# Optimization experiments

Measured on AMD Instinct MI355X. Metric: run time of the kernel, lower is better.

## Reference

```python
import jax, jax.numpy as jnp
import numpy as np

EPS = 1e-5

def _dynconv(x, w):
    # x: [B,C,H,W], w: [B,O,C,1,1] -> per-sample 1x1 conv == batched matmul
    return jnp.einsum('bchw,boc->bohw', x, w[:, :, :, 0, 0])

def _instance_norm(x):
    # InstanceNorm2d(affine=False): normalize over HxW per (b,c), biased var
    m = jnp.mean(x, axis=(2, 3), keepdims=True)
    v = jnp.var(x, axis=(2, 3), keepdims=True)
    return (x - m) / jnp.sqrt(v + EPS)

def setup_inputs() -> dict:
    key = jax.random.key(0)
    ks = jax.random.split(key, 10)
    B, C, O = 16, 128, 128
    hs = [128, 64, 32, 16, 8]
    inp = {}
    for i, h in enumerate(hs):
        inp[f'x{i+1}'] = jax.random.normal(ks[i], (B, C, h, h), dtype=jnp.float32)
        inp[f'l{i+1}fs'] = jax.random.normal(ks[5 + i], (B, O, C, 1, 1), dtype=jnp.float32)
    return inp

def reference(x1, x2, x3, x4, x5, l1fs, l2fs, l3fs, l4fs, l5fs):
    y1 = _instance_norm(_dynconv(x1, l1fs))
    y2 = _instance_norm(_dynconv(x2, l2fs))
    y3 = _instance_norm(_dynconv(x3, l3fs))
    y4 = _instance_norm(_dynconv(x4, l4fs))
    y5 = _dynconv(x5, l5fs)  # x5 is not normalized in the original
    return (y1, y2, y3, y4, y5)
```

## Files before the change

kernel.cpp:

```cpp
#include <hip/hip_runtime.h>
#include <hip/hip_bf16.h>

typedef float f32x4 __attribute__((ext_vector_type(4)));
typedef short s16x8 __attribute__((ext_vector_type(8)));
typedef short s16x4 __attribute__((ext_vector_type(4)));

static __device__ __forceinline__ short f2bf(float f) {
  union { __hip_bfloat16 h; short s; } u;
  u.h = __float2bfloat16(f);
  return u.s;
}
static __device__ __forceinline__ float bf2f(short s) {
  union { unsigned u; float f; } v;
  v.u = ((unsigned)(unsigned short)s) << 16;
  return v.f;
}
static __device__ __forceinline__ unsigned pack2(float a, float b) {
  return ((unsigned)(unsigned short)f2bf(a)) | (((unsigned)(unsigned short)f2bf(b)) << 16);
}
static __device__ __forceinline__ s16x8 pack8(f32x4 v0, f32x4 v1) {
  s16x8 r;
  r[0] = f2bf(v0.x); r[1] = f2bf(v0.y); r[2] = f2bf(v0.z); r[3] = f2bf(v0.w);
  r[4] = f2bf(v1.x); r[5] = f2bf(v1.y); r[6] = f2bf(v1.z); r[7] = f2bf(v1.w);
  return r;
}

#define GRAW_SZ   (4 * 16 * 16384)
#define MX_BASE   GRAW_SZ
#define MX_SZ     (4 * 16 * 128)
#define MEAN_BASE (MX_BASE + MX_SZ)
#define RSTD_BASE (MEAN_BASE + MX_SZ)

__global__ __launch_bounds__(256, 3) void k_gram(
    const float* __restrict__ x0, const float* __restrict__ x1,
    const float* __restrict__ x2, const float* __restrict__ x3,
    float* __restrict__ graw, float* __restrict__ mxraw) {
  const int bid = blockIdx.x;
  const float* xp; int s, b, ch, L; long long N;
  if (bid < 512)      { s = 0; b = bid >> 5; ch = bid & 31; xp = x0; N = 16384; L = 512; }
  else if (bid < 640) { int r = bid - 512; s = 1; b = r >> 3; ch = r & 7; xp = x1; N = 4096; L = 512; }
  else if (bid < 672) { int r = bid - 640; s = 2; b = r >> 1; ch = r & 1; xp = x2; N = 1024; L = 512; }
  else                { int r = bid - 672; s = 3; b = r;      ch = 0;     xp = x3; N = 256;  L = 256; }
  const int nsc = L >> 7;
  const int t = threadIdx.x;
  const int lane = t & 63, wv = t >> 6;
  const int wm = wv >> 1, wn = wv & 1;
  const int l15 = lane & 15, quad = lane >> 4;

  __shared__ short Xs[128 * 136];

  f32x4 acc[4][4];
  #pragma unroll
  for (int i = 0; i < 4; ++i)
    #pragma unroll
    for (int j = 0; j < 4; ++j) { f32x4 z = {0.f,0.f,0.f,0.f}; acc[i][j] = z; }
  float mxp[4] = {0.f, 0.f, 0.f, 0.f};

  const float* xb = xp + (long long)b * 128 * N + (long long)ch * L;

  for (int sc = 0; sc < nsc; ++sc) {
    if (sc) __syncthreads();
    {
      const int cg = t >> 5, kq = t & 31;
      const float* gp = xb + (long long)sc * 128 + (long long)cg * N + (kq << 2);
      short* lsp = &Xs[cg * 136 + (kq << 2)];
      #pragma unroll
      for (int it = 0; it < 16; ++it) {
        f32x4 v = *(const f32x4*)gp;
        s16x4 sv; sv[0]=f2bf(v.x); sv[1]=f2bf(v.y); sv[2]=f2bf(v.z); sv[3]=f2bf(v.w);
        *(s16x4*)lsp = sv;
        gp += (long long)8 * N;
        lsp += 8 * 136;
      }
    }
    __syncthreads();
    #pragma unroll
    for (int r4 = 0; r4 < 4; ++r4) {
      const int k0 = (r4 << 5) + (quad << 3);
      s16x8 af[4], bfq[4];
      #pragma unroll
      for (int i = 0; i < 4; ++i)
        af[i] = *(const s16x8*)&Xs[(wm * 64 + i * 16 + l15) * 136 + k0];
      if (wn == 0) {
        #pragma unroll
        for (int i = 0; i < 4; ++i) {
          float sum8 = 0.f;
          #pragma unroll
          for (int k = 0; k < 8; ++k) sum8 += bf2f(af[i][k]);
          mxp[i] += sum8;
        }
      }
      if (wm == wn) {
        #pragma unroll
        for (int j = 0; j < 4; ++j) bfq[j] = af[j];
      } else {
        #pragma unroll
        for (int j = 0; j < 4; ++j)
          bfq[j] = *(const s16x8*)&Xs[(wn * 64 + j * 16 + l15) * 136 + k0];
      }
      #pragma unroll
      for (int i = 0; i < 4; ++i)
        #pragma unroll
        for (int j = 0; j < 4; ++j)
          acc[i][j] = __builtin_amdgcn_mfma_f32_16x16x32_bf16(af[i], bfq[j], acc[i][j], 0, 0, 0);
    }
  }

  float* G = graw + (long long)(s * 16 + b) * 16384;
  #pragma unroll
  for (int i = 0; i < 4; ++i) {
    #pragma unroll
    for (int rr = 0; rr < 4; ++rr) {
      const int row = wm * 64 + i * 16 + quad * 4 + rr;
      #pragma unroll
      for (int j = 0; j < 4; ++j) {
        const int col = wn * 64 + j * 16 + l15;
        unsafeAtomicAdd(&G[row * 128 + col], acc[i][j][rr]);
      }
    }
  }
  #pragma unroll
  for (int i = 0; i < 4; ++i) {
    mxp[i] += __shfl_xor(mxp[i], 16, 64);
    mxp[i] += __shfl_xor(mxp[i], 32, 64);
  }
  if (wn == 0 && quad == 0) {
    float* MX = mxraw + (long long)(s * 16 + b) * 128;
    #pragma unroll
    for (int i = 0; i < 4; ++i)
      unsafeAtomicAdd(&MX[wm * 64 + i * 16 + l15], mxp[i]);
  }
}

__global__ __launch_bounds__(256) void k_stats(
    const float* __restrict__ l0, const float* __restrict__ l1,
    const float* __restrict__ l2, const float* __restrict__ l3,
    const float* __restrict__ graw, const float* __restrict__ mxraw,
    float* __restrict__ meanw, float* __restrict__ rstdw) {
  const int bid = blockIdx.x;
  const int s = bid >> 6, rm = bid & 63, b = rm >> 2, og = rm & 3;
  const float* lp = (s == 0) ? l0 : (s == 1) ? l1 : (s == 2) ? l2 : l3;
  const float Ninv = (s == 0) ? (1.f/16384.f) : (s == 1) ? (1.f/4096.f)
                   : (s == 2) ? (1.f/1024.f) : (1.f/256.f);
  const int t = threadIdx.x;

  __shared__ short Gs[16384];
  __shared__ float wl[32 * 132];
  __shared__ float mxl[128];
  __shared__ float red[4][32];
  __shared__ float meanb[32];

  const float* Gg = graw + (long long)(s * 16 + b) * 16384;
  #pragma unroll
  for (int jj = 0; jj < 16; ++jj) {
    const int F = jj * 256 + t;
    const int c = F >> 5, c4 = F & 31;
    f32x4 v = *(const f32x4*)(Gg + F * 4);
    const int q = c4 >> 1, half = c4 & 1;
    s16x4 sv; sv.x = f2bf(v.x); sv.y = f2bf(v.y); sv.z = f2bf(v.z); sv.w = f2bf(v.w);
    *(s16x4*)&Gs[c * 128 + ((q ^ (c & 15)) << 3) + half * 4] = sv;
  }
  const float* wg = lp + ((long long)b * 128 + og * 32) * 128;
  #pragma unroll
  for (int jj = 0; jj < 4; ++jj) {
    const int F = jj * 256 + t;
    const int o = F >> 5, c4 = F & 31;
    *(f32x4*)&wl[o * 132 + c4 * 4] = *(const f32x4*)(wg + F * 4);
  }
  if (t < 32) *(f32x4*)&mxl[t * 4] =
      *(const f32x4*)(mxraw + (long long)(s * 16 + b) * 128 + t * 4);
  __syncthreads();

  const int lane = t & 63, wv = t >> 6;
  const int oslot = lane >> 3, c8 = lane & 7;
  float e2a[4] = {0.f, 0.f, 0.f, 0.f};
  #pragma unroll
  for (int qq = 0; qq < 4; ++qq) {
    const int q = wv * 4 + qq;
    float wr[4][8];
    #pragma unroll
    for (int r = 0; r < 4; ++r) {
      f32x4 w0 = *(const f32x4*)&wl[(oslot + 8 * r) * 132 + q * 8];
      f32x4 w1 = *(const f32x4*)&wl[(oslot + 8 * r) * 132 + q * 8 + 4];
      wr[r][0]=w0.x; wr[r][1]=w0.y; wr[r][2]=w0.z; wr[r][3]=w0.w;
      wr[r][4]=w1.x; wr[r][5]=w1.y; wr[r][6]=w1.z; wr[r][7]=w1.w;
    }
    #pragma unroll
    for (int ci = 0; ci < 16; ++ci) {
      const int c = c8 + 8 * ci;
      s16x8 gv = *(const s16x8*)&Gs[c * 128 + ((q ^ (c & 15)) << 3)];
      float gf[8];
      #pragma unroll
      for (int k = 0; k < 8; ++k) gf[k] = bf2f(gv[k]);
      #pragma unroll
      for (int r = 0; r < 4; ++r) {
        float inner = 0.f;
        #pragma unroll
        for (int k = 0; k < 8; ++k) inner += wr[r][k] * gf[k];
        e2a[r] += wl[(oslot + 8 * r) * 132 + c] * inner;
      }
    }
  }
  float mn[4] = {0.f, 0.f, 0.f, 0.f};
  if (wv == 0) {
    #pragma unroll
    for (int ci = 0; ci < 16; ++ci) {
      const int c = c8 + 8 * ci;
      const float mxc = mxl[c];
      #pragma unroll
      for (int r = 0; r < 4; ++r) mn[r] += wl[(oslot + 8 * r) * 132 + c] * mxc;
    }
  }
  #pragma unroll
  for (int off = 1; off < 8; off <<= 1) {
    #pragma unroll
    for (int r = 0; r < 4; ++r) {
      e2a[r] += __shfl_xor(e2a[r], off, 64);
      mn[r]  += __shfl_xor(mn[r], off, 64);
    }
  }
  if (c8 == 0) {
    #pragma unroll
    for (int r = 0; r < 4; ++r) {
      red[wv][oslot + 8 * r] = e2a[r];
      if (wv == 0) meanb[oslot + 8 * r] = mn[r];
    }
  }
  __syncthreads();
  if (t < 32) {
    const float e2 = (red[0][t] + red[1][t] + red[2][t] + red[3][t]) * Ninv;
    const float mean = meanb[t] * Ninv;
    const float var = e2 - mean * mean;
    const float rstd = rsqrtf(var + 1e-5f);
    const int idx = (s * 16 + b) * 128 + og * 32 + t;
    meanw[idx] = mean;
    rstdw[idx] = rstd;
  }
}

__global__ __launch_bounds__(256, 3) void k_gemm(
    const float* __restrict__ x0, const float* __restrict__ x1,
    const float* __restrict__ x2, const float* __restrict__ x3,
    const float* __restrict__ x4,
    const float* __restrict__ l0, const float* __restrict__ l1,
    const float* __restrict__ l2, const float* __restrict__ l3,
    const float* __restrict__ l4,
    const float* __restrict__ meanw, const float* __restrict__ rstdw,
    float* __restrict__ out) {
  const int bid = blockIdx.x;
  int s, b, nt; const float *xp, *lp; int N; long long ooff;
  if (bid < 2048)      { s = 0; b = bid >> 7;            nt = bid & 127;     xp = x0; lp = l0; N = 16384; ooff = 0; }
  else if (bid < 2560) { int r = bid - 2048; s = 1; b = r >> 5; nt = r & 31; xp = x1; lp = l1; N = 4096;  ooff = 33554432LL; }
  else if (bid < 2688) { int r = bid - 2560; s = 2; b = r >> 3; nt = r & 7;  xp = x2; lp = l2; N = 1024;  ooff = 41943040LL; }
  else if (bid < 2720) { int r = bid - 2688; s = 3; b = r >> 1; nt = r & 1;  xp = x3; lp = l3; N = 256;   ooff = 44040192LL; }
  else                 { int r = bid - 2720; s = 4; b = r;      nt = 0;      xp = x4; lp = l4; N = 64;    ooff = 44564480LL; }
  const int t = threadIdx.x;
  const int lane = t & 63, wv = t >> 6;

  __shared__ short Xt[128 * 136];

  {
    const int g = lane >> 2, q4 = lane & 3;
    const float* xg = xp + (long long)b * 128 * N + (long long)nt * 128;
    #pragma unroll
    for (int j = 0; j < 16; ++j) {
      const int cb = (j & 7) * 16 + wv * 4;
      const int c  = cb + q4;
      const int n0 = (j >> 3) * 64 + g * 4;
      f32x4 v = {0.f, 0.f, 0.f, 0.f};
      if (nt * 128 + n0 + 3 < N)
        v = *(const f32x4*)(xg + (long long)c * N + n0);
      unsigned u01 = pack2(v.x, v.y);
      unsigned u23 = pack2(v.z, v.w);
      unsigned p01 = __shfl_xor(u01, 1, 64);
      unsigned p23 = __shfl_xor(u23, 1, 64);
      unsigned t01 = (q4 & 1) ? ((p01 >> 16) | (u01 & 0xffff0000u))
                              : ((u01 & 0xffffu) | (p01 << 16));
      unsigned t23 = (q4 & 1) ? ((p23 >> 16) | (u23 & 0xffff0000u))
                              : ((u23 & 0xffffu) | (p23 << 16));
      unsigned s01 = __shfl_xor(t01, 2, 64);
      unsigned s23 = __shfl_xor(t23, 2, 64);
      unsigned lo = (q4 & 2) ? s23 : t01;
      unsigned hi = (q4 & 2) ? t23 : s01;
      const int n = n0 + q4;
      *(unsigned long long*)&Xt[n * 136 + cb] =
          ((unsigned long long)hi << 32) | (unsigned long long)lo;
    }
  }
  __syncthreads();

  const int wm = wv >> 1, wn = wv & 1;
  const int l15 = lane & 15, quad = lane >> 4;
  const float* wg = lp + (long long)b * 16384;
  f32x4 acc[4][4];
  #pragma unroll
  for (int i = 0; i < 4; ++i)
    #pragma unroll
    for (int j = 0; j < 4; ++j) { f32x4 z = {0.f,0.f,0.f,0.f}; acc[i][j] = z; }

  #pragma unroll
  for (int kk = 0; kk < 4; ++kk) {
    s16x8 af[4], bfq[4];
    #pragma unroll
    for (int i = 0; i < 4; ++i) {
      const int m = wm * 64 + i * 16 + l15;
      f32x4 w0 = *(const f32x4*)(wg + m * 128 + kk * 32 + quad * 8);
      f32x4 w1 = *(const f32x4*)(wg + m * 128 + kk * 32 + quad * 8 + 4);
      af[i] = pack8(w0, w1);
    }
    #pragma unroll
    for (int j = 0; j < 4; ++j) {
      const int n = wn * 64 + j * 16 + l15;
      bfq[j] = *(const s16x8*)&Xt[n * 136 + kk * 32 + quad * 8];
    }
    #pragma unroll
    for (int i = 0; i < 4; ++i)
      #pragma unroll
      for (int j = 0; j < 4; ++j)
        acc[i][j] = __builtin_amdgcn_mfma_f32_16x16x32_bf16(af[i], bfq[j], acc[i][j], 0, 0, 0);
  }

  const int sb = (s * 16 + b) * 128;
  #pragma unroll
  for (int i = 0; i < 4; ++i) {
    #pragma unroll
    for (int rr = 0; rr < 4; ++rr) {
      const int o = wm * 64 + i * 16 + quad * 4 + rr;
      float mean = 0.f, rstd = 1.f;
      if (s < 4) { mean = meanw[sb + o]; rstd = rstdw[sb + o]; }
      float* orow = out + ooff + (long long)(b * 128 + o) * N + (long long)nt * 128;
      #pragma unroll
      for (int j = 0; j < 4; ++j) {
        const int n = wn * 64 + j * 16 + l15;
        if (nt * 128 + n < N) orow[n] = (acc[i][j][rr] - mean) * rstd;
      }
    }
  }
}

extern "C" void kernel_launch(void* const* d_in, const int* in_sizes, int n_in,
                              void* d_out, int out_size, void* d_ws, size_t ws_size,
                              hipStream_t stream) {
  const float* x[5] = {(const float*)d_in[0], (const float*)d_in[2], (const float*)d_in[4],
                       (const float*)d_in[6], (const float*)d_in[8]};
  const float* l[5] = {(const float*)d_in[1], (const float*)d_in[3], (const float*)d_in[5],
                       (const float*)d_in[7], (const float*)d_in[9]};
  float* ws  = (float*)d_ws;
  float* out = (float*)d_out;

  hipMemsetAsync(d_ws, 0, (size_t)(GRAW_SZ + MX_SZ) * sizeof(float), stream);

  k_gram <<<688,  256, 0, stream>>>(x[0], x[1], x[2], x[3], ws, ws + MX_BASE);
  k_stats<<<256,  256, 0, stream>>>(l[0], l[1], l[2], l[3], ws, ws + MX_BASE,
                                    ws + MEAN_BASE, ws + RSTD_BASE);
  k_gemm <<<2736, 256, 0, stream>>>(x[0], x[1], x[2], x[3], x[4],
                                    l[0], l[1], l[2], l[3], l[4],
                                    ws + MEAN_BASE, ws + RSTD_BASE, out);
}
```

Before: 451.4 us.

## Swizzle LDS tiles without padding, double gram split count, raise occupancy bounds

After: 580.7 us. +28.7%, slower.

```diff
diff --git a/kernel.cpp b/kernel.cpp
--- a/kernel.cpp
+++ b/kernel.cpp
@@ -31,23 +31,22 @@
 #define MEAN_BASE (MX_BASE + MX_SZ)
 #define RSTD_BASE (MEAN_BASE + MX_SZ)
 
-__global__ __launch_bounds__(256, 3) void k_gram(
+__global__ __launch_bounds__(256, 5) void k_gram(
     const float* __restrict__ x0, const float* __restrict__ x1,
     const float* __restrict__ x2, const float* __restrict__ x3,
     float* __restrict__ graw, float* __restrict__ mxraw) {
   const int bid = blockIdx.x;
-  const float* xp; int s, b, ch, L; long long N;
-  if (bid < 512)      { s = 0; b = bid >> 5; ch = bid & 31; xp = x0; N = 16384; L = 512; }
-  else if (bid < 640) { int r = bid - 512; s = 1; b = r >> 3; ch = r & 7; xp = x1; N = 4096; L = 512; }
-  else if (bid < 672) { int r = bid - 640; s = 2; b = r >> 1; ch = r & 1; xp = x2; N = 1024; L = 512; }
-  else                { int r = bid - 672; s = 3; b = r;      ch = 0;     xp = x3; N = 256;  L = 256; }
-  const int nsc = L >> 7;
+  const float* xp; int s, b, ch; long long N;
+  if (bid < 1024)      { s = 0; b = bid >> 6; ch = bid & 63; xp = x0; N = 16384; }
+  else if (bid < 1280) { int r = bid - 1024; s = 1; b = r >> 4; ch = r & 15; xp = x1; N = 4096; }
+  else if (bid < 1344) { int r = bid - 1280; s = 2; b = r >> 2; ch = r & 3;  xp = x2; N = 1024; }
+  else                 { int r = bid - 1344; s = 3; b = r;      ch = 0;      xp = x3; N = 256;  }
   const int t = threadIdx.x;
   const int lane = t & 63, wv = t >> 6;
   const int wm = wv >> 1, wn = wv & 1;
   const int l15 = lane & 15, quad = lane >> 4;
 
-  __shared__ short Xs[128 * 136];
+  __shared__ short Xs[128 * 128];
 
   f32x4 acc[4][4];
   #pragma unroll
@@ -56,31 +55,32 @@
     for (int j = 0; j < 4; ++j) { f32x4 z = {0.f,0.f,0.f,0.f}; acc[i][j] = z; }
   float mxp[4] = {0.f, 0.f, 0.f, 0.f};
 
-  const float* xb = xp + (long long)b * 128 * N + (long long)ch * L;
-
-  for (int sc = 0; sc < nsc; ++sc) {
+  const float* xb = xp + (long long)b * 128 * N + (long long)ch * 256;
+
+  #pragma unroll
+  for (int sc = 0; sc < 2; ++sc) {
     if (sc) __syncthreads();
     {
       const int cg = t >> 5, kq = t & 31;
       const float* gp = xb + (long long)sc * 128 + (long long)cg * N + (kq << 2);
-      short* lsp = &Xs[cg * 136 + (kq << 2)];
       #pragma unroll
       for (int it = 0; it < 16; ++it) {
+        const int row = cg + (it << 3);
         f32x4 v = *(const f32x4*)gp;
         s16x4 sv; sv[0]=f2bf(v.x); sv[1]=f2bf(v.y); sv[2]=f2bf(v.z); sv[3]=f2bf(v.w);
-        *(s16x4*)lsp = sv;
+        *(s16x4*)&Xs[row * 128 + (((kq >> 1) ^ (row & 15)) << 3) + ((kq & 1) << 2)] = sv;
         gp += (long long)8 * N;
-        lsp += 8 * 136;
       }
     }
     __syncthreads();
     #pragma unroll
     for (int r4 = 0; r4 < 4; ++r4) {
-      const int k0 = (r4 << 5) + (quad << 3);
       s16x8 af[4], bfq[4];
       #pragma unroll
-      for (int i = 0; i < 4; ++i)
-        af[i] = *(const s16x8*)&Xs[(wm * 64 + i * 16 + l15) * 136 + k0];
+      for (int i = 0; i < 4; ++i) {
+        const int m = wm * 64 + i * 16 + l15;
+        af[i] = *(const s16x8*)&Xs[m * 128 + (((r4 * 4 + quad) ^ (m & 15)) << 3)];
+      }
       if (wn == 0) {
         #pragma unroll
         for (int i = 0; i < 4; ++i) {
@@ -95,8 +95,10 @@
         for (int j = 0; j < 4; ++j) bfq[j] = af[j];
       } else {
         #pragma unroll
-        for (int j = 0; j < 4; ++j)
-          bfq[j] = *(const s16x8*)&Xs[(wn * 64 + j * 16 + l15) * 136 + k0];
+        for (int j = 0; j < 4; ++j) {
+          const int n = wn * 64 + j * 16 + l15;
+          bfq[j] = *(const s16x8*)&Xs[n * 128 + (((r4 * 4 + quad) ^ (n & 15)) << 3)];
+        }
       }
       #pragma unroll
       for (int i = 0; i < 4; ++i)
@@ -238,7 +240,7 @@
   }
 }
 
-__global__ __launch_bounds__(256, 3) void k_gemm(
+__global__ __launch_bounds__(256, 5) void k_gemm(
     const float* __restrict__ x0, const float* __restrict__ x1,
     const float* __restrict__ x2, const float* __restrict__ x3,
     const float* __restrict__ x4,
@@ -257,7 +259,7 @@
   const int t = threadIdx.x;
   const int lane = t & 63, wv = t >> 6;
 
-  __shared__ short Xt[128 * 136];
+  __shared__ short Xt[128 * 128];
 
   {
     const int g = lane >> 2, q4 = lane & 3;
@@ -283,7 +285,8 @@
       unsigned lo = (q4 & 2) ? s23 : t01;
       unsigned hi = (q4 & 2) ? t23 : s01;
       const int n = n0 + q4;
-      *(unsigned long long*)&Xt[n * 136 + cb] =
+      const int chunk = cb >> 3, hoff = cb & 7;
+      *(unsigned long long*)&Xt[n * 128 + ((chunk ^ (n & 15)) << 3) + hoff] =
           ((unsigned long long)hi << 32) | (unsigned long long)lo;
     }
   }
@@ -311,7 +314,7 @@
     #pragma unroll
     for (int j = 0; j < 4; ++j) {
       const int n = wn * 64 + j * 16 + l15;
-      bfq[j] = *(const s16x8*)&Xt[n * 136 + kk * 32 + quad * 8];
+      bfq[j] = *(const s16x8*)&Xt[n * 128 + (((kk * 4 + quad) ^ (n & 15)) << 3)];
     }
     #pragma unroll
     for (int i = 0; i < 4; ++i)
@@ -350,7 +353,7 @@
 
   hipMemsetAsync(d_ws, 0, (size_t)(GRAW_SZ + MX_SZ) * sizeof(float), stream);
 
-  k_gram <<<688,  256, 0, stream>>>(x[0], x[1], x[2], x[3], ws, ws + MX_BASE);
+  k_gram <<<1360, 256, 0, stream>>>(x[0], x[1], x[2], x[3], ws, ws + MX_BASE);
   k_stats<<<256,  256, 0, stream>>>(l[0], l[1], l[2], l[3], ws, ws + MX_BASE,
                                     ws + MEAN_BASE, ws + RSTD_BASE);
   k_gemm <<<2736, 256, 0, stream>>>(x[0], x[1], x[2], x[3], x[4],
```
